# Kernel tuning notes

Hardware: AMD Instinct MI355X
Metric: run time of the kernel (lower is better)

## Reference

```python
import jax, jax.numpy as jnp
import numpy as np

B, T, N_EMBED, HEAD_SIZE = 512, 256, 384, 64

def setup_inputs() -> dict:
    key = jax.random.key(0)
    k1, k2, k3, k4 = jax.random.split(key, 4)
    x = jax.random.normal(k1, (B, T, N_EMBED), dtype=jnp.float32)
    # nn.Linear(n_embed, head_size, bias=False) weights, stored as [in, out] for x @ W
    scale = 1.0 / np.sqrt(N_EMBED)
    Wk = jax.random.uniform(k2, (N_EMBED, HEAD_SIZE), jnp.float32, -scale, scale)
    Wq = jax.random.uniform(k3, (N_EMBED, HEAD_SIZE), jnp.float32, -scale, scale)
    Wv = jax.random.uniform(k4, (N_EMBED, HEAD_SIZE), jnp.float32, -scale, scale)
    return {"x": x, "Wk": Wk, "Wq": Wq, "Wv": Wv}

def reference(x, Wk, Wq, Wv):
    # Single causal self-attention head (dropout in eval mode / identity)
    k = x @ Wk  # [B, T, H]
    q = x @ Wq
    v = x @ Wv
    wei = jnp.einsum('bth,bsh->bts', q, k) * (HEAD_SIZE ** -0.5)  # [B, T, T]
    causal = jnp.tril(jnp.ones((T, T), dtype=bool))
    wei = jnp.where(causal, wei, -jnp.inf)
    wei = jax.nn.softmax(wei, axis=-1)
    out = jnp.einsum('bts,bsh->bth', wei, v)  # [B, T, H]
    return out
```

## Files before the change

kernel.cpp:

```cpp
#include <hip/hip_runtime.h>
#include <stdint.h>


typedef short s16x8 __attribute__((ext_vector_type(8)));
typedef short s16x4 __attribute__((ext_vector_type(4)));
typedef float f32x4 __attribute__((ext_vector_type(4)));

#define LOG2E_OVER_8 0.18033688011112042f

__device__ inline short f2bf(float f) {
  union { float f; uint32_t u; } v; v.f = f;
  uint32_t r = (v.u + 0x7fffu + ((v.u >> 16) & 1u)) >> 16;
  return (short)r;
}

__global__ __launch_bounds__(256) void prep_w(const float* __restrict__ Wk,
                                              const float* __restrict__ Wq,
                                              const float* __restrict__ Wv,
                                              short* __restrict__ Wt2) {
  int idx = blockIdx.x * 256 + threadIdx.x;
  int kk = idx & 31;
  int n = (idx >> 5) % 192;
  int kc = idx / (32 * 192);
  int col = n & 63;
  int w = n >> 6;
  const float* W = (w == 0) ? Wk : (w == 1) ? Wq : Wv;
  float v = W[(kc * 32 + kk) * 64 + col];
  if (w == 1) v *= LOG2E_OVER_8;
  Wt2[idx] = f2bf(v);
}

__global__ __launch_bounds__(512, 2) void fused_head(const float* __restrict__ x,
                                                     const short* __restrict__ Wt2,
                                                     float* __restrict__ out) {
  __shared__ __align__(16) short Xs[64 * 392];
  __shared__ __align__(16) short Kls[256 * 72];
  __shared__ __align__(16) short Qls[256 * 72];
  __shared__ __align__(16) short Vt[64 * 264];

  const int tid = threadIdx.x;
  const int wave = tid >> 6;
  const int lane = tid & 63;
  const int l15 = lane & 15;
  const int quad = lane >> 4;
  const int b = blockIdx.x;
  const float* xb = x + (long)b * (256 * 384);

  const int rt = wave >> 1;
  const int nh = wave & 1;
  const short* wbase = Wt2 + (nh * 96 + l15) * 32 + quad * 8;

  for (int ch = 0; ch < 4; ++ch) {
    const int R0 = ch * 64;
#pragma unroll
    for (int j = 0; j < 12; ++j) {
      int slot = tid + j * 512;
      int row = slot / 96;
      int c4 = slot - row * 96;
      f32x4 a = *(const f32x4*)(xb + (R0 + row) * 384 + c4 * 4);
      s16x4 h;
      h[0] = f2bf(a[0]); h[1] = f2bf(a[1]); h[2] = f2bf(a[2]); h[3] = f2bf(a[3]);
      *(s16x4*)&Xs[row * 392 + c4 * 4] = h;
    }
    __syncthreads();

    f32x4 acc[6];
#pragma unroll
    for (int nt = 0; nt < 6; ++nt) acc[nt] = (f32x4)0.0f;
    const short* abase = &Xs[(rt * 16 + l15) * 392 + quad * 8];
#pragma unroll 2
    for (int kc = 0; kc < 12; ++kc) {
      s16x8 af = *(const s16x8*)(abase + kc * 32);
#pragma unroll
      for (int nt = 0; nt < 6; ++nt) {
        s16x8 bf = *(const s16x8*)(wbase + kc * 6144 + nt * 512);
        acc[nt] = __builtin_amdgcn_mfma_f32_16x16x32_bf16(af, bf, acc[nt], 0, 0, 0);
      }
    }

    const int srow = R0 + rt * 16 + quad * 4;
#pragma unroll
    for (int nt = 0; nt < 6; ++nt) {
      const int gn = nh * 6 + nt;
      if (gn < 4) {
        const int col = gn * 16 + l15;
#pragma unroll
        for (int r = 0; r < 4; ++r) Kls[(srow + r) * 72 + col] = f2bf(acc[nt][r]);
      } else if (gn < 8) {
        const int col = (gn - 4) * 16 + l15;
#pragma unroll
        for (int r = 0; r < 4; ++r) Qls[(srow + r) * 72 + col] = f2bf(acc[nt][r]);
      } else {
        const int hcol = (gn - 8) * 16 + l15;
#pragma unroll
        for (int r = 0; r < 4; ++r) Vt[hcol * 264 + srow + r] = f2bf(acc[nt][r]);
      }
    }
    __syncthreads();
  }

  short* Psw = Xs + wave * (16 * 72);

  for (int ti = 0; ti < 2; ++ti) {
    const int t = ti ? (15 - wave) : wave;
    const int q0 = t * 16;

    s16x8 qf0 = *(const s16x8*)&Qls[(q0 + l15) * 72 + quad * 8];
    s16x8 qf1 = *(const s16x8*)&Qls[(q0 + l15) * 72 + 32 + quad * 8];

    f32x4 Oacc[4];
#pragma unroll
    for (int n = 0; n < 4; ++n) Oacc[n] = (f32x4)0.0f;
    float mrow[4] = {-1e30f, -1e30f, -1e30f, -1e30f};
    float lrow[4] = {0.f, 0.f, 0.f, 0.f};

    const int nchunks = (t >> 2) + 1;
    for (int c = 0; c < nchunks; ++c) {
      const int s0 = c * 64;
      f32x4 S[4];
#pragma unroll
      for (int n = 0; n < 4; ++n) {
        s16x8 kf0 = *(const s16x8*)&Kls[(s0 + n * 16 + l15) * 72 + quad * 8];
        s16x8 kf1 = *(const s16x8*)&Kls[(s0 + n * 16 + l15) * 72 + 32 + quad * 8];
        f32x4 z = (f32x4)0.0f;
        z = __builtin_amdgcn_mfma_f32_16x16x32_bf16(qf0, kf0, z, 0, 0, 0);
        z = __builtin_amdgcn_mfma_f32_16x16x32_bf16(qf1, kf1, z, 0, 0, 0);
        S[n] = z;
      }
      if (c == nchunks - 1) {
#pragma unroll
        for (int n = 0; n < 4; ++n) {
          const int s_abs = s0 + n * 16 + l15;
#pragma unroll
          for (int r = 0; r < 4; ++r) {
            const int q_abs = q0 + quad * 4 + r;
            if (s_abs > q_abs) S[n][r] = -1e30f;
          }
        }
      }

      float alpha[4];
#pragma unroll
      for (int r = 0; r < 4; ++r) {
        float mx = fmaxf(fmaxf(S[0][r], S[1][r]), fmaxf(S[2][r], S[3][r]));
        mx = fmaxf(mx, __shfl_xor(mx, 1));
        mx = fmaxf(mx, __shfl_xor(mx, 2));
        mx = fmaxf(mx, __shfl_xor(mx, 4));
        mx = fmaxf(mx, __shfl_xor(mx, 8));
        float mnew = fmaxf(mrow[r], mx);
        alpha[r] = __builtin_amdgcn_exp2f(mrow[r] - mnew);
        mrow[r] = mnew;
      }
      float rs[4] = {0.f, 0.f, 0.f, 0.f};
#pragma unroll
      for (int n = 0; n < 4; ++n) {
#pragma unroll
        for (int r = 0; r < 4; ++r) {
          float p = __builtin_amdgcn_exp2f(S[n][r] - mrow[r]);
          rs[r] += p;
          Psw[(quad * 4 + r) * 72 + n * 16 + l15] = f2bf(p);
        }
      }
#pragma unroll
      for (int r = 0; r < 4; ++r) {
        float s = rs[r];
        s += __shfl_xor(s, 1);
        s += __shfl_xor(s, 2);
        s += __shfl_xor(s, 4);
        s += __shfl_xor(s, 8);
        lrow[r] = lrow[r] * alpha[r] + s;
#pragma unroll
        for (int n = 0; n < 4; ++n) Oacc[n][r] *= alpha[r];
      }
      asm volatile("s_waitcnt lgkmcnt(0)" ::: "memory");

      s16x8 pf0 = *(const s16x8*)&Psw[l15 * 72 + quad * 8];
      s16x8 pf1 = *(const s16x8*)&Psw[l15 * 72 + 32 + quad * 8];
#pragma unroll
      for (int n = 0; n < 4; ++n) {
        s16x8 vf0 = *(const s16x8*)&Vt[(n * 16 + l15) * 264 + s0 + quad * 8];
        s16x8 vf1 = *(const s16x8*)&Vt[(n * 16 + l15) * 264 + s0 + 32 + quad * 8];
        Oacc[n] = __builtin_amdgcn_mfma_f32_16x16x32_bf16(pf0, vf0, Oacc[n], 0, 0, 0);
        Oacc[n] = __builtin_amdgcn_mfma_f32_16x16x32_bf16(pf1, vf1, Oacc[n], 0, 0, 0);
      }
    }

    float inv[4];
#pragma unroll
    for (int r = 0; r < 4; ++r) inv[r] = 1.0f / lrow[r];
    float* ob = out + ((long)b * 256 + q0 + quad * 4) * 64;
#pragma unroll
    for (int n = 0; n < 4; ++n)
#pragma unroll
      for (int r = 0; r < 4; ++r)
        ob[r * 64 + n * 16 + l15] = Oacc[n][r] * inv[r];
  }
}

extern "C" void kernel_launch(void* const* d_in, const int* in_sizes, int n_in,
                              void* d_out, int out_size, void* d_ws, size_t ws_size,
                              hipStream_t stream) {
  const float* x = (const float*)d_in[0];
  const float* Wk = (const float*)d_in[1];
  const float* Wq = (const float*)d_in[2];
  const float* Wv = (const float*)d_in[3];
  float* out = (float*)d_out;
  short* Wt2 = (short*)d_ws;

  prep_w<<<288, 256, 0, stream>>>(Wk, Wq, Wv, Wt2);
  fused_head<<<512, 512, 0, stream>>>(x, Wt2, out);
}
```

Measured before the change: 357.3 us.

## Restructure fused attention head into 1024-thread blocks with MFMA-fragment LDS layouts

The kernel now runs 16 waves per block. The QKV projection is restructured to stream K-chunks of x and weights through LDS, with register prefetch of the next chunk, and each wave computes a 4x3 MFMA tile. K, Q, V, P and the weights are stored in fragment-native (pre-swizzled) LDS layouts, so each operand is a single contiguous 16-byte load per lane. The attention phase gives one 16-row query tile per wave and processes keys in 128-wide blocks while skipping fully masked key tiles. The trade-offs are higher LDS use (160 KB), only one block per CU, and uneven causal work across waves inside a block.

```diff
diff --git a/kernel.cpp b/kernel.cpp
--- a/kernel.cpp
+++ b/kernel.cpp
@@ -17,26 +17,33 @@
 __global__ __launch_bounds__(256) void prep_w(const float* __restrict__ Wk,
                                               const float* __restrict__ Wq,
                                               const float* __restrict__ Wv,
-                                              short* __restrict__ Wt2) {
+                                              short* __restrict__ Wt3) {
   int idx = blockIdx.x * 256 + threadIdx.x;
-  int kk = idx & 31;
-  int n = (idx >> 5) % 192;
-  int kc = idx / (32 * 192);
+  int j = idx & 7;
+  int lane = (idx >> 3) & 63;
+  int rest = idx >> 9;
+  int ntile = rest % 12;
+  int kc = rest / 12;
+  int n = ntile * 16 + (lane & 15);
+  int kk = (lane >> 4) * 8 + j;
   int col = n & 63;
   int w = n >> 6;
   const float* W = (w == 0) ? Wk : (w == 1) ? Wq : Wv;
   float v = W[(kc * 32 + kk) * 64 + col];
   if (w == 1) v *= LOG2E_OVER_8;
-  Wt2[idx] = f2bf(v);
-}
-
-__global__ __launch_bounds__(512, 2) void fused_head(const float* __restrict__ x,
-                                                     const short* __restrict__ Wt2,
-                                                     float* __restrict__ out) {
-  __shared__ __align__(16) short Xs[64 * 392];
-  __shared__ __align__(16) short Kls[256 * 72];
-  __shared__ __align__(16) short Qls[256 * 72];
-  __shared__ __align__(16) short Vt[64 * 264];
+  Wt3[idx] = f2bf(v);
+}
+
+__global__ __launch_bounds__(1024) void fused_head(const float* __restrict__ x,
+                                                   const short* __restrict__ Wt3,
+                                                   float* __restrict__ out) {
+  __shared__ __align__(16) short LDS[81920];
+  short* Kf = LDS;
+  short* Qf = LDS + 16384;
+  short* Vf = LDS + 32768;
+  short* Pb = LDS + 49152;
+  short* Xc = LDS + 49152;
+  short* Wsl = LDS + 49152 + 8192;
 
   const int tid = threadIdx.x;
   const int wave = tid >> 6;
@@ -46,155 +53,180 @@
   const int b = blockIdx.x;
   const float* xb = x + (long)b * (256 * 384);
 
-  const int rt = wave >> 1;
-  const int nh = wave & 1;
-  const short* wbase = Wt2 + (nh * 96 + l15) * 32 + quad * 8;
-
-  for (int ch = 0; ch < 4; ++ch) {
-    const int R0 = ch * 64;
-#pragma unroll
-    for (int j = 0; j < 12; ++j) {
-      int slot = tid + j * 512;
-      int row = slot / 96;
-      int c4 = slot - row * 96;
-      f32x4 a = *(const f32x4*)(xb + (R0 + row) * 384 + c4 * 4);
-      s16x4 h;
-      h[0] = f2bf(a[0]); h[1] = f2bf(a[1]); h[2] = f2bf(a[2]); h[3] = f2bf(a[3]);
-      *(s16x4*)&Xs[row * 392 + c4 * 4] = h;
-    }
+  const int mgrp = wave >> 2;
+  const int ngrp = wave & 3;
+
+  const int m0s = tid >> 3;
+  const int kq0 = (tid & 7) * 4;
+  const int xoff0 = m0s * 384 + kq0;
+  const int xoff1 = xoff0 + 128 * 384;
+  const int lds0 = (m0s >> 4) * 512 + ((m0s & 15) + (kq0 >> 3) * 16) * 8 + (kq0 & 7);
+  const int lds1 = lds0 + 8 * 512;
+  const bool wact = (tid < 768);
+
+  f32x4 acc[4][3];
+#pragma unroll
+  for (int i = 0; i < 4; ++i)
+#pragma unroll
+    for (int k2 = 0; k2 < 3; ++k2) acc[i][k2] = (f32x4)0.0f;
+
+  f32x4 xa0 = *(const f32x4*)(xb + xoff0);
+  f32x4 xa1 = *(const f32x4*)(xb + xoff1);
+  s16x8 wv;
+  if (wact) wv = *(const s16x8*)(Wt3 + tid * 8);
+
+  for (int kc = 0; kc < 12; ++kc) {
     __syncthreads();
-
-    f32x4 acc[6];
-#pragma unroll
-    for (int nt = 0; nt < 6; ++nt) acc[nt] = (f32x4)0.0f;
-    const short* abase = &Xs[(rt * 16 + l15) * 392 + quad * 8];
-#pragma unroll 2
-    for (int kc = 0; kc < 12; ++kc) {
-      s16x8 af = *(const s16x8*)(abase + kc * 32);
-#pragma unroll
-      for (int nt = 0; nt < 6; ++nt) {
-        s16x8 bf = *(const s16x8*)(wbase + kc * 6144 + nt * 512);
-        acc[nt] = __builtin_amdgcn_mfma_f32_16x16x32_bf16(af, bf, acc[nt], 0, 0, 0);
-      }
-    }
-
-    const int srow = R0 + rt * 16 + quad * 4;
-#pragma unroll
-    for (int nt = 0; nt < 6; ++nt) {
-      const int gn = nh * 6 + nt;
-      if (gn < 4) {
-        const int col = gn * 16 + l15;
-#pragma unroll
-        for (int r = 0; r < 4; ++r) Kls[(srow + r) * 72 + col] = f2bf(acc[nt][r]);
-      } else if (gn < 8) {
-        const int col = (gn - 4) * 16 + l15;
-#pragma unroll
-        for (int r = 0; r < 4; ++r) Qls[(srow + r) * 72 + col] = f2bf(acc[nt][r]);
-      } else {
-        const int hcol = (gn - 8) * 16 + l15;
-#pragma unroll
-        for (int r = 0; r < 4; ++r) Vt[hcol * 264 + srow + r] = f2bf(acc[nt][r]);
-      }
-    }
+    s16x4 h0, h1;
+    h0[0] = f2bf(xa0[0]); h0[1] = f2bf(xa0[1]); h0[2] = f2bf(xa0[2]); h0[3] = f2bf(xa0[3]);
+    h1[0] = f2bf(xa1[0]); h1[1] = f2bf(xa1[1]); h1[2] = f2bf(xa1[2]); h1[3] = f2bf(xa1[3]);
+    *(s16x4*)(Xc + lds0) = h0;
+    *(s16x4*)(Xc + lds1) = h1;
+    if (wact) *(s16x8*)(Wsl + tid * 8) = wv;
     __syncthreads();
+    if (kc < 11) {
+      xa0 = *(const f32x4*)(xb + xoff0 + (kc + 1) * 32);
+      xa1 = *(const f32x4*)(xb + xoff1 + (kc + 1) * 32);
+      if (wact) wv = *(const s16x8*)(Wt3 + (kc + 1) * 6144 + tid * 8);
+    }
+    s16x8 af[4];
+#pragma unroll
+    for (int i = 0; i < 4; ++i)
+      af[i] = *(const s16x8*)(Xc + (mgrp * 4 + i) * 512 + lane * 8);
+#pragma unroll
+    for (int k2 = 0; k2 < 3; ++k2) {
+      s16x8 bfv = *(const s16x8*)(Wsl + (ngrp * 3 + k2) * 512 + lane * 8);
+#pragma unroll
+      for (int i = 0; i < 4; ++i)
+        acc[i][k2] = __builtin_amdgcn_mfma_f32_16x16x32_bf16(af[i], bfv, acc[i][k2], 0, 0, 0);
+    }
   }
 
-  short* Psw = Xs + wave * (16 * 72);
-
-  for (int ti = 0; ti < 2; ++ti) {
-    const int t = ti ? (15 - wave) : wave;
-    const int q0 = t * 16;
-
-    s16x8 qf0 = *(const s16x8*)&Qls[(q0 + l15) * 72 + quad * 8];
-    s16x8 qf1 = *(const s16x8*)&Qls[(q0 + l15) * 72 + 32 + quad * 8];
-
-    f32x4 Oacc[4];
-#pragma unroll
-    for (int n = 0; n < 4; ++n) Oacc[n] = (f32x4)0.0f;
-    float mrow[4] = {-1e30f, -1e30f, -1e30f, -1e30f};
-    float lrow[4] = {0.f, 0.f, 0.f, 0.f};
-
-    const int nchunks = (t >> 2) + 1;
-    for (int c = 0; c < nchunks; ++c) {
-      const int s0 = c * 64;
-      f32x4 S[4];
-#pragma unroll
-      for (int n = 0; n < 4; ++n) {
-        s16x8 kf0 = *(const s16x8*)&Kls[(s0 + n * 16 + l15) * 72 + quad * 8];
-        s16x8 kf1 = *(const s16x8*)&Kls[(s0 + n * 16 + l15) * 72 + 32 + quad * 8];
+#pragma unroll
+  for (int i = 0; i < 4; ++i) {
+    const int rowb = (mgrp * 4 + i) * 16 + quad * 4;
+#pragma unroll
+    for (int k2 = 0; k2 < 3; ++k2) {
+      const int nt = ngrp * 3 + k2;
+      const int h = (nt * 16 + l15) & 63;
+      const int which = nt >> 2;
+#pragma unroll
+      for (int r = 0; r < 4; ++r) {
+        const short v = f2bf(acc[i][k2][r]);
+        const int row = rowb + r;
+        if (which == 0)
+          Kf[((row >> 4) * 2 + (h >> 5)) * 512 + ((row & 15) + ((h & 31) >> 3) * 16) * 8 + (h & 7)] = v;
+        else if (which == 1)
+          Qf[((row >> 4) * 2 + (h >> 5)) * 512 + ((row & 15) + ((h & 31) >> 3) * 16) * 8 + (h & 7)] = v;
+        else
+          Vf[((row >> 5) * 4 + (h >> 4)) * 512 + ((h & 15) + ((row & 31) >> 3) * 16) * 8 + (row & 7)] = v;
+      }
+    }
+  }
+  __syncthreads();
+
+  const int t = wave;
+  const int q0 = t * 16;
+  short* Pw = Pb + wave * 2048;
+
+  s16x8 qf0 = *(const s16x8*)(Qf + (t * 2 + 0) * 512 + lane * 8);
+  s16x8 qf1 = *(const s16x8*)(Qf + (t * 2 + 1) * 512 + lane * 8);
+
+  f32x4 Oacc[4];
+#pragma unroll
+  for (int n = 0; n < 4; ++n) Oacc[n] = (f32x4)0.0f;
+  float mrow[4] = {-1e30f, -1e30f, -1e30f, -1e30f};
+  float lrow[4] = {0.f, 0.f, 0.f, 0.f};
+
+  const int nb = (t >= 8) ? 2 : 1;
+  for (int cb = 0; cb < nb; ++cb) {
+    const int st0 = cb * 8;
+    const bool last = (cb == nb - 1);
+    const int nuse = last ? (t - cb * 8 + 1) : 8;
+
+    float S[8][4];
+#pragma unroll
+    for (int n = 0; n < 8; ++n) {
+      if (n < nuse) {
+        s16x8 kf0 = *(const s16x8*)(Kf + ((st0 + n) * 2 + 0) * 512 + lane * 8);
+        s16x8 kf1 = *(const s16x8*)(Kf + ((st0 + n) * 2 + 1) * 512 + lane * 8);
         f32x4 z = (f32x4)0.0f;
         z = __builtin_amdgcn_mfma_f32_16x16x32_bf16(qf0, kf0, z, 0, 0, 0);
         z = __builtin_amdgcn_mfma_f32_16x16x32_bf16(qf1, kf1, z, 0, 0, 0);
-        S[n] = z;
-      }
-      if (c == nchunks - 1) {
-#pragma unroll
-        for (int n = 0; n < 4; ++n) {
-          const int s_abs = s0 + n * 16 + l15;
+        if (last) {
+          const int s_abs = cb * 128 + n * 16 + l15;
 #pragma unroll
           for (int r = 0; r < 4; ++r) {
             const int q_abs = q0 + quad * 4 + r;
-            if (s_abs > q_abs) S[n][r] = -1e30f;
+            S[n][r] = (s_abs > q_abs) ? -1e30f : z[r];
           }
+        } else {
+#pragma unroll
+          for (int r = 0; r < 4; ++r) S[n][r] = z[r];
         }
-      }
-
-      float alpha[4];
+      } else {
+#pragma unroll
+        for (int r = 0; r < 4; ++r) S[n][r] = -1e30f;
+      }
+    }
+
+    float alpha[4];
+#pragma unroll
+    for (int r = 0; r < 4; ++r) {
+      float mx = S[0][r];
+#pragma unroll
+      for (int n = 1; n < 8; ++n) mx = fmaxf(mx, S[n][r]);
+      mx = fmaxf(mx, __shfl_xor(mx, 1));
+      mx = fmaxf(mx, __shfl_xor(mx, 2));
+      mx = fmaxf(mx, __shfl_xor(mx, 4));
+      mx = fmaxf(mx, __shfl_xor(mx, 8));
+      float mnew = fmaxf(mrow[r], mx);
+      alpha[r] = __builtin_amdgcn_exp2f(mrow[r] - mnew);
+      mrow[r] = mnew;
+    }
+    float rs[4] = {0.f, 0.f, 0.f, 0.f};
+#pragma unroll
+    for (int n = 0; n < 8; ++n) {
 #pragma unroll
       for (int r = 0; r < 4; ++r) {
-        float mx = fmaxf(fmaxf(S[0][r], S[1][r]), fmaxf(S[2][r], S[3][r]));
-        mx = fmaxf(mx, __shfl_xor(mx, 1));
-        mx = fmaxf(mx, __shfl_xor(mx, 2));
-        mx = fmaxf(mx, __shfl_xor(mx, 4));
-        mx = fmaxf(mx, __shfl_xor(mx, 8));
-        float mnew = fmaxf(mrow[r], mx);
-        alpha[r] = __builtin_amdgcn_exp2f(mrow[r] - mnew);
-        mrow[r] = mnew;
-      }
-      float rs[4] = {0.f, 0.f, 0.f, 0.f};
-#pragma unroll
-      for (int n = 0; n < 4; ++n) {
-#pragma unroll
-        for (int r = 0; r < 4; ++r) {
-          float p = __builtin_amdgcn_exp2f(S[n][r] - mrow[r]);
-          rs[r] += p;
-          Psw[(quad * 4 + r) * 72 + n * 16 + l15] = f2bf(p);
-        }
-      }
-#pragma unroll
-      for (int r = 0; r < 4; ++r) {
-        float s = rs[r];
-        s += __shfl_xor(s, 1);
-        s += __shfl_xor(s, 2);
-        s += __shfl_xor(s, 4);
-        s += __shfl_xor(s, 8);
-        lrow[r] = lrow[r] * alpha[r] + s;
-#pragma unroll
-        for (int n = 0; n < 4; ++n) Oacc[n][r] *= alpha[r];
-      }
-      asm volatile("s_waitcnt lgkmcnt(0)" ::: "memory");
-
-      s16x8 pf0 = *(const s16x8*)&Psw[l15 * 72 + quad * 8];
-      s16x8 pf1 = *(const s16x8*)&Psw[l15 * 72 + 32 + quad * 8];
-#pragma unroll
-      for (int n = 0; n < 4; ++n) {
-        s16x8 vf0 = *(const s16x8*)&Vt[(n * 16 + l15) * 264 + s0 + quad * 8];
-        s16x8 vf1 = *(const s16x8*)&Vt[(n * 16 + l15) * 264 + s0 + 32 + quad * 8];
-        Oacc[n] = __builtin_amdgcn_mfma_f32_16x16x32_bf16(pf0, vf0, Oacc[n], 0, 0, 0);
-        Oacc[n] = __builtin_amdgcn_mfma_f32_16x16x32_bf16(pf1, vf1, Oacc[n], 0, 0, 0);
-      }
-    }
-
-    float inv[4];
-#pragma unroll
-    for (int r = 0; r < 4; ++r) inv[r] = 1.0f / lrow[r];
-    float* ob = out + ((long)b * 256 + q0 + quad * 4) * 64;
-#pragma unroll
-    for (int n = 0; n < 4; ++n)
-#pragma unroll
-      for (int r = 0; r < 4; ++r)
-        ob[r * 64 + n * 16 + l15] = Oacc[n][r] * inv[r];
+        float p = __builtin_amdgcn_exp2f(S[n][r] - mrow[r]);
+        rs[r] += p;
+        Pw[(n >> 1) * 512 + ((quad * 4 + r) + ((n & 1) * 2 + (l15 >> 3)) * 16) * 8 + (l15 & 7)] = f2bf(p);
+      }
+    }
+#pragma unroll
+    for (int r = 0; r < 4; ++r) {
+      float s = rs[r];
+      s += __shfl_xor(s, 1);
+      s += __shfl_xor(s, 2);
+      s += __shfl_xor(s, 4);
+      s += __shfl_xor(s, 8);
+      lrow[r] = lrow[r] * alpha[r] + s;
+#pragma unroll
+      for (int n = 0; n < 4; ++n) Oacc[n][r] *= alpha[r];
+    }
+    asm volatile("s_waitcnt lgkmcnt(0)" ::: "memory");
+
+    const int kblks = (nuse + 1) >> 1;
+    for (int sb = 0; sb < kblks; ++sb) {
+      s16x8 pf = *(const s16x8*)(Pw + sb * 512 + lane * 8);
+#pragma unroll
+      for (int n2 = 0; n2 < 4; ++n2) {
+        s16x8 vfv = *(const s16x8*)(Vf + ((cb * 4 + sb) * 4 + n2) * 512 + lane * 8);
+        Oacc[n2] = __builtin_amdgcn_mfma_f32_16x16x32_bf16(pf, vfv, Oacc[n2], 0, 0, 0);
+      }
+    }
   }
+
+  float inv[4];
+#pragma unroll
+  for (int r = 0; r < 4; ++r) inv[r] = 1.0f / lrow[r];
+  float* ob = out + ((long)b * 256 + q0 + quad * 4) * 64;
+#pragma unroll
+  for (int n = 0; n < 4; ++n)
+#pragma unroll
+    for (int r = 0; r < 4; ++r)
+      ob[r * 64 + n * 16 + l15] = Oacc[n][r] * inv[r];
 }
 
 extern "C" void kernel_launch(void* const* d_in, const int* in_sizes, int n_in,
@@ -205,8 +237,8 @@
   const float* Wq = (const float*)d_in[2];
   const float* Wv = (const float*)d_in[3];
   float* out = (float*)d_out;
-  short* Wt2 = (short*)d_ws;
-
-  prep_w<<<288, 256, 0, stream>>>(Wk, Wq, Wv, Wt2);
-  fused_head<<<512, 512, 0, stream>>>(x, Wt2, out);
-}
+  short* Wt3 = (short*)d_ws;
+
+  prep_w<<<288, 256, 0, stream>>>(Wk, Wq, Wv, Wt3);
+  fused_head<<<512, 1024, 0, stream>>>(x, Wt3, out);
+}
```

New measurement: 318.5 us. -10.9%, faster.
